# Optimization experiments

Measured on AMD Instinct MI355X. Metric: run time of the kernel, lower is better.

The kernel has to match this reference:

```python
import jax, jax.numpy as jnp
import numpy as np

# ---- constants from train_cfg / hardcoded voxel_resolution dicts ----
PC_MIN_X, PC_MIN_Y, PC_MIN_Z = -51.2, -51.2, -5.0
VX, VY, VZ = 0.1, 0.1, 0.2          # voxel_size
OSF = 8                              # out_size_factor
OVERLAP = 0.1                        # gaussian_overlap
MIN_RADIUS = 2
GX, GY, GZ = 128, 128, 2             # heatmap grid (0.8m xy, 4m z steps)
STEP_XY, STEP_Z = 0.4, 1.0           # inner-loop voxel_resolution steps
FMAP = 128                           # feature_map_size = 1024 // 8
EPS32 = float(np.finfo(np.float32).eps)


def gaussian_radius(h, w, min_overlap=OVERLAP):
    # mmdet3d CornerNet-style radius (note the /2, not /(2a))
    b1 = h + w
    c1 = w * h * (1 - min_overlap) / (1 + min_overlap)
    r1 = (b1 + jnp.sqrt(jnp.maximum(b1 * b1 - 4.0 * c1, 0.0))) / 2.0
    b2 = 2.0 * (h + w)
    c2 = (1 - min_overlap) * w * h
    r2 = (b2 + jnp.sqrt(jnp.maximum(b2 * b2 - 16.0 * c2, 0.0))) / 2.0
    b3 = -2.0 * min_overlap * (h + w)
    c3 = (min_overlap - 1.0) * w * h
    r3 = (b3 + jnp.sqrt(jnp.maximum(b3 * b3 - 16.0 * min_overlap * c3, 0.0))) / 2.0
    return jnp.minimum(jnp.minimum(r1, r2), r3)


def build_heatmap(boxes):
    # boxes: [N,9] = (x, y, z_gravity, w, l, h, yaw, vx, vy); labels only route
    # boxes into tasks (task_num=1 here -> all boxes drawn, cls_id unused).
    # N << max_objs*dense_reg (=500) so the cap never triggers.
    x, y, z = boxes[:, 0], boxes[:, 1], boxes[:, 2]
    wf = boxes[:, 3] / VX / OSF   # width  in feature-map units
    lf = boxes[:, 4] / VY / OSF   # length in feature-map units
    hf = boxes[:, 5] / VZ / OSF   # height in feature-map units

    r_xy = gaussian_radius(lf, wf)
    r_z = jnp.maximum(gaussian_radius(lf, hf), gaussian_radius(wf, hf))
    # int() truncation, then clamp by min_radius
    rx = jnp.maximum(MIN_RADIUS, jnp.trunc(r_xy / STEP_XY).astype(jnp.int32))
    ry = rx
    rz = jnp.maximum(MIN_RADIUS, jnp.trunc(r_z / STEP_Z).astype(jnp.int32))

    cx = (x - (-51.2)) / STEP_XY
    cy = (y - (-51.2)) / STEP_XY
    cz = (z - (-5.0)) / STEP_Z
    cxi = cx.astype(jnp.int32)  # trunc-toward-zero, as torch .to(int32)
    cyi = cy.astype(jnp.int32)
    czi = cz.astype(jnp.int32)

    valid = (wf > 0) & (lf > 0) \
        & (cxi >= 0) & (cxi < FMAP) & (cyi >= 0) & (cyi < FMAP) \
        & (czi >= 0) & (czi <= GZ - 1)

    # gaussian sigmas per axis: diameter/6
    sx = (2.0 * rx.astype(jnp.float32) + 1.0) / 6.0
    sy = (2.0 * ry.astype(jnp.float32) + 1.0) / 6.0
    sz = (2.0 * rz.astype(jnp.float32) + 1.0) / 6.0

    dx = jnp.arange(GX, dtype=jnp.int32)[None, :] - cxi[:, None]   # [N,GX]
    dy = jnp.arange(GY, dtype=jnp.int32)[None, :] - cyi[:, None]   # [N,GY]
    dz = jnp.arange(GZ, dtype=jnp.int32)[None, :] - czi[:, None]   # [N,GZ]

    ex = dx.astype(jnp.float32) ** 2 / (2.0 * sx[:, None] ** 2)
    ey = dy.astype(jnp.float32) ** 2 / (2.0 * sy[:, None] ** 2)
    ez = dz.astype(jnp.float32) ** 2 / (2.0 * sz[:, None] ** 2)
    g = jnp.exp(-(ex[:, :, None, None] + ey[:, None, :, None] + ez[:, None, None, :]))
    g = jnp.where(g < EPS32, 0.0, g)  # eps zeroing as in mmdet gaussianND

    win = (jnp.abs(dx) <= rx[:, None])[:, :, None, None] \
        & (jnp.abs(dy) <= ry[:, None])[:, None, :, None] \
        & (jnp.abs(dz) <= rz[:, None])[:, None, None, :]
    g = g * win * valid[:, None, None, None]
    return jnp.max(g, axis=0)  # [GX,GY,GZ]; scatter-max over objects


def lin_resize(x, axis, out_size):
    # 1D linear resize, pytorch trilinear align_corners=False semantics
    in_size = x.shape[axis]
    scale = in_size / out_size
    coords = (jnp.arange(out_size, dtype=jnp.float32) + 0.5) * scale - 0.5
    coords = jnp.clip(coords, 0.0, in_size - 1)
    lo = jnp.floor(coords).astype(jnp.int32)
    hi = jnp.minimum(lo + 1, in_size - 1)
    w = coords - lo.astype(jnp.float32)
    shape = [1] * x.ndim
    shape[axis] = out_size
    w = w.reshape(shape)
    return jnp.take(x, lo, axis=axis) * (1.0 - w) + jnp.take(x, hi, axis=axis) * w


def align(voxels, conv_w, conv_b, out_shape):
    # 1x1x1 Conv3d 64->128 (student has 64 ch), then trilinear interp
    v = jnp.einsum('bcdhw,oc->bodhw', voxels, conv_w) + conv_b[None, :, None, None, None]
    v = lin_resize(v, 2, out_shape[0])
    v = lin_resize(v, 3, out_shape[1])
    v = lin_resize(v, 4, out_shape[2])
    return v


def setup_inputs() -> dict:
    key = jax.random.key(0)
    k1, k2, k3, k4, k5, k6, k7, k8, k9 = jax.random.split(key, 9)
    N = 100
    xy = jax.random.uniform(k1, (N, 2), minval=-50.0, maxval=-1.0)
    z = jax.random.uniform(k2, (N, 1), minval=-5.0, maxval=-3.2)
    dims = jax.random.uniform(k3, (N, 3), minval=1.5, maxval=8.0)
    rest = jax.random.normal(k4, (N, 3)) * 0.1
    gt_bboxes_3d = jnp.concatenate([xy, z, dims, rest], axis=1)  # [N,9]
    gt_labels_3d = jax.random.randint(k5, (N,), 0, 3)
    teacher = jax.random.normal(k6, (1, 128, 2, 128, 128), dtype=jnp.float32)
    student = jax.random.normal(k7, (1, 64, 8, 256, 256), dtype=jnp.float32)
    conv_w = jax.random.normal(k8, (128, 64), dtype=jnp.float32) * 0.125
    conv_b = jax.random.normal(k9, (128,), dtype=jnp.float32) * 0.01
    return {"gt_bboxes_3d": gt_bboxes_3d, "gt_labels_3d": gt_labels_3d,
            "teacher_voxel_feats": teacher, "student_voxel_feats": student,
            "conv_w": conv_w, "conv_b": conv_b}


def reference(gt_bboxes_3d, gt_labels_3d, teacher_voxel_feats, student_voxel_feats, conv_w, conv_b):
    hm = build_heatmap(gt_bboxes_3d)                 # [128,128,2]
    # stack per sample -> [1,B,128,128,2] -> permute(0,1,4,2,3) -> [1,1,2,128,128]
    hm3d = jnp.transpose(hm, (2, 0, 1))[None, None]
    s = align(student_voxel_feats, conv_w, conv_b, teacher_voxel_feats.shape[2:])
    loss = jnp.abs(s - teacher_voxel_feats) * hm3d   # L1, reduction='none'
    loss = loss / (hm3d.sum() + 1e-4)
    return loss * 10.0
```

## Files before the change

### kernel.cpp

```cpp
#include <hip/hip_runtime.h>
#include <math.h>

#define EPS32 1.1920928955078125e-07f
#define NSP 32768
#define HB 128
#define PB 4096


__device__ __forceinline__ float gauss_radius(float h, float w) {
#pragma clang fp contract(off)
    const float mo = 0.1f;
    float b1 = h + w;
    float c1 = w * h * (1.0f - mo) / (1.0f + mo);
    float r1 = (b1 + sqrtf(fmaxf(b1 * b1 - 4.0f * c1, 0.0f))) / 2.0f;
    float b2 = 2.0f * (h + w);
    float c2 = (1.0f - mo) * w * h;
    float r2 = (b2 + sqrtf(fmaxf(b2 * b2 - 16.0f * c2, 0.0f))) / 2.0f;
    float b3 = -2.0f * mo * (h + w);
    float c3 = (mo - 1.0f) * w * h;
    float r3 = (b3 + sqrtf(fmaxf(b3 * b3 - 16.0f * mo * c3, 0.0f))) / 2.0f;
    return fminf(fminf(r1, r2), r3);
}

__global__ void k_stage1(const float* __restrict__ boxes, int N,
                         const float* __restrict__ S,
                         float* __restrict__ P,
                         float* __restrict__ hmv,
                         float* __restrict__ partial) {
    int bx = blockIdx.x;
    int tid = threadIdx.x;

    if (bx < HB) {
        __shared__ int   s_cxi[128], s_cyi[128], s_czi[128], s_rx[128], s_rz[128];
        __shared__ float s_ix[128], s_iz[128];
        if (tid < N) {
#pragma clang fp contract(off)
            int b = tid;
            float x = boxes[b * 9 + 0];
            float y = boxes[b * 9 + 1];
            float z = boxes[b * 9 + 2];
            float wf = boxes[b * 9 + 3] / 0.1f / 8.0f;
            float lf = boxes[b * 9 + 4] / 0.1f / 8.0f;
            float hf = boxes[b * 9 + 5] / 0.2f / 8.0f;
            float r_xy = gauss_radius(lf, wf);
            float r_z  = fmaxf(gauss_radius(lf, hf), gauss_radius(wf, hf));
            int rx = max(2, (int)truncf(r_xy / 0.4f));
            int rz = max(2, (int)truncf(r_z / 1.0f));
            float cx = (x + 51.2f) / 0.4f;
            float cy = (y + 51.2f) / 0.4f;
            float cz = (z + 5.0f) / 1.0f;
            int cxi = (int)cx, cyi = (int)cy, czi = (int)cz;
            int valid = (wf > 0.0f) && (lf > 0.0f) &&
                        cxi >= 0 && cxi < 128 && cyi >= 0 && cyi < 128 &&
                        czi >= 0 && czi <= 1;
            float sx = (2.0f * (float)rx + 1.0f) / 6.0f;
            float sz = (2.0f * (float)rz + 1.0f) / 6.0f;
            s_cxi[b] = cxi;
            s_cyi[b] = cyi;
            s_czi[b] = czi;
            s_rx[b]  = valid ? rx : -1;
            s_rz[b]  = rz;
            s_ix[b]  = 1.0f / (2.0f * sx * sx);
            s_iz[b]  = 1.0f / (2.0f * sz * sz);
        }
        __syncthreads();

        int i = bx * 256 + tid;
        int y = i & 127, x = (i >> 7) & 127, zc = i >> 14;
        float m = 0.0f;
        for (int b = 0; b < N; ++b) {
            int rx = s_rx[b];
            int dx = x - s_cxi[b];
            if (dx > rx || dx < -rx) continue;
            int dy = y - s_cyi[b];
            if (dy > rx || dy < -rx) continue;
            int rz = s_rz[b];
            int dz = zc - s_czi[b];
            if (dz > rz || dz < -rz) continue;
            float e = (float)(dx * dx + dy * dy) * s_ix[b]
                    + (float)(dz * dz) * s_iz[b];
            float g = expf(-e);
            if (g >= EPS32) m = fmaxf(m, g);
        }
        hmv[i] = m;
        __shared__ float sm[256];
        sm[tid] = m;
        __syncthreads();
        for (int s = 128; s > 0; s >>= 1) {
            if (tid < s) sm[tid] += sm[tid + s];
            __syncthreads();
        }
        if (tid == 0) partial[bx] = sm[0];
    } else {
        int j = (bx - HB) * 256 + tid;
        int wp = j & 63;
        int h  = (j >> 6) & 127;
        int d  = (j >> 13) & 1;
        int c  = j >> 14;
        int zl = d ? 5 : 1;
        const float4* S4 = (const float4*)S;
        long base = ((long)(c * 8 + zl) * 256 + 2 * h) * 64 + wp;
        float4 a = S4[base];
        float4 b = S4[base + 64];
        float4 e = S4[base + 16384];
        float4 f = S4[base + 16384 + 64];
        float2 r;
        r.x = (((a.x + a.y) + (b.x + b.y)) + ((e.x + e.y) + (f.x + f.y))) * 0.125f;
        r.y = (((a.z + a.w) + (b.z + b.w)) + ((e.z + e.w) + (f.z + f.w))) * 0.125f;
        ((float2*)P)[j] = r;
    }
}

__global__ void k_final(const float* __restrict__ P, const float* __restrict__ T,
                        const float* __restrict__ W, const float* __restrict__ Bb,
                        const float* __restrict__ hmv, const float* __restrict__ partial,
                        float* __restrict__ out) {
    __shared__ float s_scale;
    int tid = threadIdx.x;
    if (tid < 64) {
        float v = partial[tid] + partial[tid + 64];
        for (int off = 32; off > 0; off >>= 1) v += __shfl_down(v, off, 64);
        if (tid == 0) s_scale = 10.0f / (v + 1e-4f);
    }
    __syncthreads();

    int s = blockIdx.x * 256 + tid;
    float p[64];
#pragma unroll
    for (int c = 0; c < 64; ++c) p[c] = P[c * NSP + s];
    float hmw = hmv[s] * s_scale;
    int o0 = blockIdx.y * 32;
#pragma unroll 4
    for (int oo = 0; oo < 32; ++oo) {
        int o = o0 + oo;
        float acc = Bb[o];
#pragma unroll
        for (int c = 0; c < 64; ++c) acc += W[o * 64 + c] * p[c];
        out[o * NSP + s] = fabsf(acc - T[o * NSP + s]) * hmw;
    }
}

__global__ void k_final_fused(const float* __restrict__ S, const float* __restrict__ T,
                              const float* __restrict__ W, const float* __restrict__ Bb,
                              const float* __restrict__ hmv, const float* __restrict__ partial,
                              float* __restrict__ out) {
    __shared__ float s_scale;
    int tid = threadIdx.x;
    if (tid < 64) {
        float v = partial[tid] + partial[tid + 64];
        for (int off = 32; off > 0; off >>= 1) v += __shfl_down(v, off, 64);
        if (tid == 0) s_scale = 10.0f / (v + 1e-4f);
    }
    __syncthreads();
    int s = blockIdx.x * 256 + tid;
    int w = s & 127, h = (s >> 7) & 127, d = s >> 14;
    int zl = d ? 5 : 1;
    const float2* S2 = (const float2*)S;
    float p[64];
#pragma unroll
    for (int c = 0; c < 64; ++c) {
        long base = ((long)(c * 8 + zl) * 256 + 2 * h) * 128 + w;
        float2 a = S2[base];
        float2 b = S2[base + 128];
        float2 e = S2[base + 32768];
        float2 f = S2[base + 32768 + 128];
        p[c] = (((a.x + a.y) + (b.x + b.y)) + ((e.x + e.y) + (f.x + f.y))) * 0.125f;
    }
    float hmw = hmv[s] * s_scale;
    int o0 = blockIdx.y * 64;
    for (int oo = 0; oo < 64; ++oo) {
        int o = o0 + oo;
        float acc = Bb[o];
#pragma unroll
        for (int c = 0; c < 64; ++c) acc += W[o * 64 + c] * p[c];
        out[o * NSP + s] = fabsf(acc - T[o * NSP + s]) * hmw;
    }
}

extern "C" void kernel_launch(void* const* d_in, const int* in_sizes, int n_in,
                              void* d_out, int out_size, void* d_ws, size_t ws_size,
                              hipStream_t stream) {
    const float* boxes   = (const float*)d_in[0];
    const float* teacher = (const float*)d_in[2];
    const float* student = (const float*)d_in[3];
    const float* conv_w  = (const float*)d_in[4];
    const float* conv_b  = (const float*)d_in[5];
    float* out = (float*)d_out;

    int N = in_sizes[0] / 9;
    if (N > 128) N = 128;

    float* wsF     = (float*)d_ws;
    float* partial = wsF;
    float* hmv     = wsF + 1024;
    float* pooled  = wsF + 65536;

    const size_t need = (size_t)(65536 + 64 * NSP) * sizeof(float);
    if (ws_size >= need) {
        k_stage1<<<HB + PB, 256, 0, stream>>>(boxes, N, student, pooled, hmv, partial);
        k_final<<<dim3(NSP / 256, 4), 256, 0, stream>>>(pooled, teacher, conv_w, conv_b,
                                                        hmv, partial, out);
    } else {
        k_stage1<<<HB, 256, 0, stream>>>(boxes, N, student,  hmv, hmv, partial);
        k_final_fused<<<dim3(NSP / 256, 2), 256, 0, stream>>>(student, teacher, conv_w, conv_b,
                                                              hmv, partial, out);
    }
}
```

Before: 249.8 us.

## Fuse pooling into register-tiled shared-memory GEMM, drop pooled intermediate

Measured after the change: 214.1 us. 1.17x faster.

```diff
diff --git a/kernel.cpp b/kernel.cpp
--- a/kernel.cpp
+++ b/kernel.cpp
@@ -4,7 +4,9 @@
 #define EPS32 1.1920928955078125e-07f
 #define NSP 32768
 #define HB 128
-#define PB 4096
+
+typedef float v4f __attribute__((ext_vector_type(4)));
+typedef float v2f __attribute__((ext_vector_type(2)));
 
 
 __device__ __forceinline__ float gauss_radius(float h, float w) {
@@ -22,158 +24,181 @@
     return fminf(fminf(r1, r2), r3);
 }
 
-__global__ void k_stage1(const float* __restrict__ boxes, int N,
-                         const float* __restrict__ S,
-                         float* __restrict__ P,
-                         float* __restrict__ hmv,
-                         float* __restrict__ partial) {
+__global__ void k_heat(const float* __restrict__ boxes, int N,
+                       float* __restrict__ hmv, float* __restrict__ partial) {
     int bx = blockIdx.x;
     int tid = threadIdx.x;
-
-    if (bx < HB) {
-        __shared__ int   s_cxi[128], s_cyi[128], s_czi[128], s_rx[128], s_rz[128];
-        __shared__ float s_ix[128], s_iz[128];
-        if (tid < N) {
+    __shared__ int   s_cxi[128], s_cyi[128], s_czi[128], s_rx[128], s_rz[128];
+    __shared__ float s_ix[128], s_iz[128];
+    if (tid < N) {
 #pragma clang fp contract(off)
-            int b = tid;
-            float x = boxes[b * 9 + 0];
-            float y = boxes[b * 9 + 1];
-            float z = boxes[b * 9 + 2];
-            float wf = boxes[b * 9 + 3] / 0.1f / 8.0f;
-            float lf = boxes[b * 9 + 4] / 0.1f / 8.0f;
-            float hf = boxes[b * 9 + 5] / 0.2f / 8.0f;
-            float r_xy = gauss_radius(lf, wf);
-            float r_z  = fmaxf(gauss_radius(lf, hf), gauss_radius(wf, hf));
-            int rx = max(2, (int)truncf(r_xy / 0.4f));
-            int rz = max(2, (int)truncf(r_z / 1.0f));
-            float cx = (x + 51.2f) / 0.4f;
-            float cy = (y + 51.2f) / 0.4f;
-            float cz = (z + 5.0f) / 1.0f;
-            int cxi = (int)cx, cyi = (int)cy, czi = (int)cz;
-            int valid = (wf > 0.0f) && (lf > 0.0f) &&
-                        cxi >= 0 && cxi < 128 && cyi >= 0 && cyi < 128 &&
-                        czi >= 0 && czi <= 1;
-            float sx = (2.0f * (float)rx + 1.0f) / 6.0f;
-            float sz = (2.0f * (float)rz + 1.0f) / 6.0f;
-            s_cxi[b] = cxi;
-            s_cyi[b] = cyi;
-            s_czi[b] = czi;
-            s_rx[b]  = valid ? rx : -1;
-            s_rz[b]  = rz;
-            s_ix[b]  = 1.0f / (2.0f * sx * sx);
-            s_iz[b]  = 1.0f / (2.0f * sz * sz);
-        }
+        int b = tid;
+        float x = boxes[b * 9 + 0];
+        float y = boxes[b * 9 + 1];
+        float z = boxes[b * 9 + 2];
+        float wf = boxes[b * 9 + 3] / 0.1f / 8.0f;
+        float lf = boxes[b * 9 + 4] / 0.1f / 8.0f;
+        float hf = boxes[b * 9 + 5] / 0.2f / 8.0f;
+        float r_xy = gauss_radius(lf, wf);
+        float r_z  = fmaxf(gauss_radius(lf, hf), gauss_radius(wf, hf));
+        int rx = max(2, (int)truncf(r_xy / 0.4f));
+        int rz = max(2, (int)truncf(r_z / 1.0f));
+        float cx = (x + 51.2f) / 0.4f;
+        float cy = (y + 51.2f) / 0.4f;
+        float cz = (z + 5.0f) / 1.0f;
+        int cxi = (int)cx, cyi = (int)cy, czi = (int)cz;
+        int valid = (wf > 0.0f) && (lf > 0.0f) &&
+                    cxi >= 0 && cxi < 128 && cyi >= 0 && cyi < 128 &&
+                    czi >= 0 && czi <= 1;
+        float sx = (2.0f * (float)rx + 1.0f) / 6.0f;
+        float sz = (2.0f * (float)rz + 1.0f) / 6.0f;
+        s_cxi[b] = cxi;
+        s_cyi[b] = cyi;
+        s_czi[b] = czi;
+        s_rx[b]  = valid ? rx : -1;
+        s_rz[b]  = rz;
+        s_ix[b]  = 1.0f / (2.0f * sx * sx);
+        s_iz[b]  = 1.0f / (2.0f * sz * sz);
+    }
+    __syncthreads();
+
+    int i = bx * 256 + tid;
+    int y = i & 127, x = (i >> 7) & 127, zc = i >> 14;
+    float m = 0.0f;
+    for (int b = 0; b < N; ++b) {
+        int rx = s_rx[b];
+        int dx = x - s_cxi[b];
+        if (dx > rx || dx < -rx) continue;
+        int dy = y - s_cyi[b];
+        if (dy > rx || dy < -rx) continue;
+        int rz = s_rz[b];
+        int dz = zc - s_czi[b];
+        if (dz > rz || dz < -rz) continue;
+        float e = (float)(dx * dx + dy * dy) * s_ix[b]
+                + (float)(dz * dz) * s_iz[b];
+        float g = expf(-e);
+        if (g >= EPS32) m = fmaxf(m, g);
+    }
+    hmv[i] = m;
+    __shared__ float sm[256];
+    sm[tid] = m;
+    __syncthreads();
+    for (int s = 128; s > 0; s >>= 1) {
+        if (tid < s) sm[tid] += sm[tid + s];
         __syncthreads();
-
-        int i = bx * 256 + tid;
-        int y = i & 127, x = (i >> 7) & 127, zc = i >> 14;
-        float m = 0.0f;
-        for (int b = 0; b < N; ++b) {
-            int rx = s_rx[b];
-            int dx = x - s_cxi[b];
-            if (dx > rx || dx < -rx) continue;
-            int dy = y - s_cyi[b];
-            if (dy > rx || dy < -rx) continue;
-            int rz = s_rz[b];
-            int dz = zc - s_czi[b];
-            if (dz > rz || dz < -rz) continue;
-            float e = (float)(dx * dx + dy * dy) * s_ix[b]
-                    + (float)(dz * dz) * s_iz[b];
-            float g = expf(-e);
-            if (g >= EPS32) m = fmaxf(m, g);
-        }
-        hmv[i] = m;
-        __shared__ float sm[256];
-        sm[tid] = m;
-        __syncthreads();
-        for (int s = 128; s > 0; s >>= 1) {
-            if (tid < s) sm[tid] += sm[tid + s];
-            __syncthreads();
-        }
-        if (tid == 0) partial[bx] = sm[0];
-    } else {
-        int j = (bx - HB) * 256 + tid;
-        int wp = j & 63;
-        int h  = (j >> 6) & 127;
-        int d  = (j >> 13) & 1;
-        int c  = j >> 14;
-        int zl = d ? 5 : 1;
-        const float4* S4 = (const float4*)S;
-        long base = ((long)(c * 8 + zl) * 256 + 2 * h) * 64 + wp;
-        float4 a = S4[base];
-        float4 b = S4[base + 64];
-        float4 e = S4[base + 16384];
-        float4 f = S4[base + 16384 + 64];
-        float2 r;
-        r.x = (((a.x + a.y) + (b.x + b.y)) + ((e.x + e.y) + (f.x + f.y))) * 0.125f;
-        r.y = (((a.z + a.w) + (b.z + b.w)) + ((e.z + e.w) + (f.z + f.w))) * 0.125f;
-        ((float2*)P)[j] = r;
-    }
-}
-
-__global__ void k_final(const float* __restrict__ P, const float* __restrict__ T,
-                        const float* __restrict__ W, const float* __restrict__ Bb,
-                        const float* __restrict__ hmv, const float* __restrict__ partial,
-                        float* __restrict__ out) {
+    }
+    if (tid == 0) partial[bx] = sm[0];
+}
+
+__global__ __launch_bounds__(256, 2)
+void k_gemm(const float* __restrict__ S, const float* __restrict__ T,
+            const float* __restrict__ W, const float* __restrict__ Bb,
+            const float* __restrict__ hmv, const float* __restrict__ partial,
+            float* __restrict__ out) {
+    __shared__ float sP[64 * 64];
+    __shared__ float sW[64 * 128];
     __shared__ float s_scale;
+
     int tid = threadIdx.x;
+    int b   = blockIdx.x;
+    int d   = b >> 8;
+    int h   = (b >> 1) & 127;
+    int w0  = (b & 1) * 64;
+    int zl  = d ? 5 : 1;
+
     if (tid < 64) {
         float v = partial[tid] + partial[tid + 64];
         for (int off = 32; off > 0; off >>= 1) v += __shfl_down(v, off, 64);
         if (tid == 0) s_scale = 10.0f / (v + 1e-4f);
     }
+
+    {
+        int o  = tid >> 1;
+        int c0 = (tid & 1) * 32;
+        const v4f* Wg = (const v4f*)(W + o * 64 + c0);
+#pragma unroll
+        for (int k = 0; k < 8; ++k) {
+            v4f wv = Wg[k];
+            int c = c0 + 4 * k;
+            sW[(c    ) * 128 + o] = wv.x;
+            sW[(c + 1) * 128 + o] = wv.y;
+            sW[(c + 2) * 128 + o] = wv.z;
+            sW[(c + 3) * 128 + o] = wv.w;
+        }
+    }
+
+    {
+#pragma unroll
+        for (int i = 0; i < 4; ++i) {
+            int Ti = tid + 256 * i;
+            int c = Ti >> 4, q = Ti & 15;
+            long base = (long)(c * 8 + zl) * 65536 + (2 * h) * 256 + 2 * (w0 + 4 * q);
+            const v4f* r0 = (const v4f*)(S + base);
+            const v4f* r1 = (const v4f*)(S + base + 256);
+            const v4f* r2 = (const v4f*)(S + base + 65536);
+            const v4f* r3 = (const v4f*)(S + base + 65536 + 256);
+            v4f a0 = __builtin_nontemporal_load(&r0[0]);
+            v4f a1 = __builtin_nontemporal_load(&r0[1]);
+            v4f b0 = __builtin_nontemporal_load(&r1[0]);
+            v4f b1 = __builtin_nontemporal_load(&r1[1]);
+            v4f e0 = __builtin_nontemporal_load(&r2[0]);
+            v4f e1 = __builtin_nontemporal_load(&r2[1]);
+            v4f f0 = __builtin_nontemporal_load(&r3[0]);
+            v4f f1 = __builtin_nontemporal_load(&r3[1]);
+            v4f pv;
+            pv.x = (((a0.x + a0.y) + (b0.x + b0.y)) + ((e0.x + e0.y) + (f0.x + f0.y))) * 0.125f;
+            pv.y = (((a0.z + a0.w) + (b0.z + b0.w)) + ((e0.z + e0.w) + (f0.z + f0.w))) * 0.125f;
+            pv.z = (((a1.x + a1.y) + (b1.x + b1.y)) + ((e1.x + e1.y) + (f1.x + f1.y))) * 0.125f;
+            pv.w = (((a1.z + a1.w) + (b1.z + b1.w)) + ((e1.z + e1.w) + (f1.z + f1.w))) * 0.125f;
+            *(v4f*)&sP[c * 64 + 4 * q] = pv;
+        }
+    }
+
     __syncthreads();
 
-    int s = blockIdx.x * 256 + tid;
-    float p[64];
-#pragma unroll
-    for (int c = 0; c < 64; ++c) p[c] = P[c * NSP + s];
-    float hmw = hmv[s] * s_scale;
-    int o0 = blockIdx.y * 32;
-#pragma unroll 4
-    for (int oo = 0; oo < 32; ++oo) {
-        int o = o0 + oo;
-        float acc = Bb[o];
-#pragma unroll
-        for (int c = 0; c < 64; ++c) acc += W[o * 64 + c] * p[c];
-        out[o * NSP + s] = fabsf(acc - T[o * NSP + s]) * hmw;
-    }
-}
-
-__global__ void k_final_fused(const float* __restrict__ S, const float* __restrict__ T,
-                              const float* __restrict__ W, const float* __restrict__ Bb,
-                              const float* __restrict__ hmv, const float* __restrict__ partial,
-                              float* __restrict__ out) {
-    __shared__ float s_scale;
-    int tid = threadIdx.x;
-    if (tid < 64) {
-        float v = partial[tid] + partial[tid + 64];
-        for (int off = 32; off > 0; off >>= 1) v += __shfl_down(v, off, 64);
-        if (tid == 0) s_scale = 10.0f / (v + 1e-4f);
-    }
-    __syncthreads();
-    int s = blockIdx.x * 256 + tid;
-    int w = s & 127, h = (s >> 7) & 127, d = s >> 14;
-    int zl = d ? 5 : 1;
-    const float2* S2 = (const float2*)S;
-    float p[64];
-#pragma unroll
+    int og = tid >> 4, sq = tid & 15;
+    int o0 = og * 8;
+
+    v4f acc[8];
+#pragma unroll
+    for (int oo = 0; oo < 8; ++oo) {
+        float bv = Bb[o0 + oo];
+        acc[oo] = (v4f){bv, bv, bv, bv};
+    }
+
+    const v4f* Pc = (const v4f*)sP;
+    const v4f* Wc = (const v4f*)sW;
+#pragma unroll 8
     for (int c = 0; c < 64; ++c) {
-        long base = ((long)(c * 8 + zl) * 256 + 2 * h) * 128 + w;
-        float2 a = S2[base];
-        float2 b = S2[base + 128];
-        float2 e = S2[base + 32768];
-        float2 f = S2[base + 32768 + 128];
-        p[c] = (((a.x + a.y) + (b.x + b.y)) + ((e.x + e.y) + (f.x + f.y))) * 0.125f;
-    }
-    float hmw = hmv[s] * s_scale;
-    int o0 = blockIdx.y * 64;
-    for (int oo = 0; oo < 64; ++oo) {
-        int o = o0 + oo;
-        float acc = Bb[o];
-#pragma unroll
-        for (int c = 0; c < 64; ++c) acc += W[o * 64 + c] * p[c];
-        out[o * NSP + s] = fabsf(acc - T[o * NSP + s]) * hmw;
+        v4f p  = Pc[c * 16 + sq];
+        v4f wa = Wc[c * 32 + og * 2];
+        v4f wb = Wc[c * 32 + og * 2 + 1];
+        acc[0] += wa.x * p;
+        acc[1] += wa.y * p;
+        acc[2] += wa.z * p;
+        acc[3] += wa.w * p;
+        acc[4] += wb.x * p;
+        acc[5] += wb.y * p;
+        acc[6] += wb.z * p;
+        acc[7] += wb.w * p;
+    }
+
+    float sc = s_scale;
+    v4f hm = *(const v4f*)&hmv[b * 64 + sq * 4];
+    v4f hw = hm * sc;
+    const v4f* T4 = (const v4f*)T;
+    v4f* O4 = (v4f*)out;
+    long base_o = (long)o0 * (NSP / 4) + b * 16 + sq;
+#pragma unroll
+    for (int oo = 0; oo < 8; ++oo) {
+        v4f tv = __builtin_nontemporal_load(&T4[base_o + (long)oo * (NSP / 4)]);
+        v4f df = acc[oo] - tv;
+        v4f r;
+        r.x = fabsf(df.x) * hw.x;
+        r.y = fabsf(df.y) * hw.y;
+        r.z = fabsf(df.z) * hw.z;
+        r.w = fabsf(df.w) * hw.w;
+        __builtin_nontemporal_store(r, &O4[base_o + (long)oo * (NSP / 4)]);
     }
 }
 
@@ -193,16 +218,8 @@
     float* wsF     = (float*)d_ws;
     float* partial = wsF;
     float* hmv     = wsF + 1024;
-    float* pooled  = wsF + 65536;
-
-    const size_t need = (size_t)(65536 + 64 * NSP) * sizeof(float);
-    if (ws_size >= need) {
-        k_stage1<<<HB + PB, 256, 0, stream>>>(boxes, N, student, pooled, hmv, partial);
-        k_final<<<dim3(NSP / 256, 4), 256, 0, stream>>>(pooled, teacher, conv_w, conv_b,
-                                                        hmv, partial, out);
-    } else {
-        k_stage1<<<HB, 256, 0, stream>>>(boxes, N, student,  hmv, hmv, partial);
-        k_final_fused<<<dim3(NSP / 256, 2), 256, 0, stream>>>(student, teacher, conv_w, conv_b,
-                                                              hmv, partial, out);
-    }
-}
+
+    k_heat<<<HB, 256, 0, stream>>>(boxes, N, hmv, partial);
+    k_gemm<<<NSP / 64, 256, 0, stream>>>(student, teacher, conv_w, conv_b,
+                                         hmv, partial, out);
+}
```
